# Kernel tuning notes

Hardware: AMD Instinct MI355X
Metric: run time of the kernel (lower is better)

## Reference

```python
import jax, jax.numpy as jnp
import numpy as np
from functools import partial

NUM_STEPS = 30  # Euler integration steps (inte_steps)


def _point_sample(vol, pts):
    """Trilinear sample of vol [C,D,H,W] at pts [N,3] (voxel coords, (d,h,w) order).
    Matches torch grid_sample(mode='bilinear', padding_mode='border', align_corners=True)
    after the normalize+flip done in PointPooling. Returns [C,N]."""
    dims = jnp.asarray(vol.shape[1:], dtype=pts.dtype)  # (D,H,W)
    p = jnp.clip(pts, 0.0, dims - 1.0)  # border padding == clamp coords
    p0 = jnp.floor(p)
    frac = p - p0  # [N,3]
    i0 = p0.astype(jnp.int32)
    i1 = jnp.minimum(i0 + 1, (dims - 1.0).astype(jnp.int32))
    d0, h0, w0 = i0[:, 0], i0[:, 1], i0[:, 2]
    d1, h1, w1 = i1[:, 0], i1[:, 1], i1[:, 2]
    fd, fh, fw = frac[:, 0], frac[:, 1], frac[:, 2]
    g = lambda d, h, w: vol[:, d, h, w]  # [C,N] gather
    c000, c001 = g(d0, h0, w0), g(d0, h0, w1)
    c010, c011 = g(d0, h1, w0), g(d0, h1, w1)
    c100, c101 = g(d1, h0, w0), g(d1, h0, w1)
    c110, c111 = g(d1, h1, w0), g(d1, h1, w1)
    c00 = c000 * (1 - fw) + c001 * fw
    c01 = c010 * (1 - fw) + c011 * fw
    c10 = c100 * (1 - fw) + c101 * fw
    c11 = c110 * (1 - fw) + c111 * fw
    c0 = c00 * (1 - fh) + c01 * fh
    c1 = c10 * (1 - fh) + c11 * fh
    return c0 * (1 - fd) + c1 * fd  # [C,N]


def _interp(flow, x):
    # flow [B,3,D,H,W], x [B,N,3] -> [B,N,3]
    out = jax.vmap(_point_sample)(flow, x)  # [B,3,N]
    return jnp.transpose(out, (0, 2, 1))


def _integrate_euler(flow, x, num_steps):
    flow = flow * (1.0 / num_steps)
    def step(x, _):
        return x + _interp(flow, x), None
    x, _ = jax.lax.scan(step, x, None, length=num_steps)
    return x


def _forward(verts, affine, flow_field):
    B, N, _ = verts.shape
    ones = jnp.ones((B, N, 1), dtype=verts.dtype)
    homog = jnp.concatenate([verts, ones], axis=-1)  # [B,N,4]
    pred = jnp.einsum('bij,bnj->bni', affine, homog)[..., :3]
    aux = _integrate_euler(flow_field, pred, NUM_STEPS)
    flow_int = aux - pred  # [B,N,3]
    pred = aux
    flow_int = jnp.transpose(flow_int, (0, 2, 1))[..., None, None]  # [B,3,N,1,1]
    homog2 = jnp.concatenate([pred, ones], axis=-1)
    inv_aff = jnp.linalg.inv(affine)
    pred = jnp.einsum('bij,bnj->bni', inv_aff, homog2)[..., :3]
    return pred, flow_int


def setup_inputs() -> dict:
    key = jax.random.key(0)
    k1, k2, k3 = jax.random.split(key, 3)
    B, N = 2, 140000
    D = H = W = 192
    dims = jnp.asarray([D - 1, H - 1, W - 1], dtype=jnp.float32)
    verts = jax.random.uniform(k1, (B, N, 3), dtype=jnp.float32) * dims
    affine = jnp.eye(4, dtype=jnp.float32)[None] + 0.01 * jax.random.normal(k2, (B, 4, 4), dtype=jnp.float32)
    flow_field = jax.random.normal(k3, (B, 3, D, H, W), dtype=jnp.float32)
    return {"verts": verts, "affine": affine, "flow_field": flow_field}


def reference(verts, affine, flow_field):
    return _forward(verts, affine, flow_field)
```

## Files before the change

### kernel.cpp

```cpp
#include <hip/hip_runtime.h>
#include <hip/hip_fp16.h>

#define NSTEPS 30
#define DIM 192
static constexpr long DHW = (long)DIM * DIM * DIM;
static constexpr int PTS_PER_WAVE = 21;

__global__ void invert4x4_kernel(const float* __restrict__ aff,
                                 float* __restrict__ out, int B) {
    int b = blockIdx.x * blockDim.x + threadIdx.x;
    if (b >= B) return;
    double a[16];
#pragma unroll
    for (int i = 0; i < 16; i++) a[i] = (double)aff[b * 16 + i];
    double s0 = a[0]*a[5]  - a[4]*a[1];
    double s1 = a[0]*a[6]  - a[4]*a[2];
    double s2 = a[0]*a[7]  - a[4]*a[3];
    double s3 = a[1]*a[6]  - a[5]*a[2];
    double s4 = a[1]*a[7]  - a[5]*a[3];
    double s5 = a[2]*a[7]  - a[6]*a[3];
    double c5 = a[10]*a[15] - a[14]*a[11];
    double c4 = a[9]*a[15]  - a[13]*a[11];
    double c3 = a[9]*a[14]  - a[13]*a[10];
    double c2 = a[8]*a[15]  - a[12]*a[11];
    double c1 = a[8]*a[14]  - a[12]*a[10];
    double c0 = a[8]*a[13]  - a[12]*a[9];
    double det = s0*c5 - s1*c4 + s2*c3 + s3*c2 - s4*c1 + s5*c0;
    double inv = 1.0 / det;
    double o[16];
    o[0]  = ( a[5]*c5 - a[6]*c4 + a[7]*c3) * inv;
    o[1]  = (-a[1]*c5 + a[2]*c4 - a[3]*c3) * inv;
    o[2]  = ( a[13]*s5 - a[14]*s4 + a[15]*s3) * inv;
    o[3]  = (-a[9]*s5 + a[10]*s4 - a[11]*s3) * inv;
    o[4]  = (-a[4]*c5 + a[6]*c2 - a[7]*c1) * inv;
    o[5]  = ( a[0]*c5 - a[2]*c2 + a[3]*c1) * inv;
    o[6]  = (-a[12]*s5 + a[14]*s2 - a[15]*s1) * inv;
    o[7]  = ( a[8]*s5 - a[10]*s2 + a[11]*s1) * inv;
    o[8]  = ( a[4]*c4 - a[5]*c2 + a[7]*c0) * inv;
    o[9]  = (-a[0]*c4 + a[1]*c2 - a[3]*c0) * inv;
    o[10] = ( a[12]*s4 - a[13]*s2 + a[15]*s0) * inv;
    o[11] = (-a[8]*s4 + a[9]*s2 - a[11]*s0) * inv;
    o[12] = (-a[4]*c3 + a[5]*c1 - a[6]*c0) * inv;
    o[13] = ( a[0]*c3 - a[1]*c1 + a[2]*c0) * inv;
    o[14] = (-a[12]*s3 + a[13]*s1 - a[14]*s0) * inv;
    o[15] = ( a[8]*s3 - a[9]*s1 + a[10]*s0) * inv;
#pragma unroll
    for (int i = 0; i < 16; i++) out[b * 16 + i] = (float)o[i];
}

__global__ __launch_bounds__(256) void repack4_kernel(const float* __restrict__ flow,
                                                      __half* __restrict__ packed) {
    long q = (long)blockIdx.x * blockDim.x + threadIdx.x;
    int b = blockIdx.y;
    long v0 = q * 4;
    if (v0 >= DHW) return;
    const float* F = flow + (size_t)b * 3 * DHW;
    float4 f0 = *reinterpret_cast<const float4*>(F + v0);
    float4 f1 = *reinterpret_cast<const float4*>(F + v0 + DHW);
    float4 f2 = *reinterpret_cast<const float4*>(F + v0 + 2 * DHW);
    union { __half2 h[2]; int2 i2; } u;
    int4 o0, o1;
    u.h[0] = __floats2half2_rn(f0.x, f1.x); u.h[1] = __floats2half2_rn(f2.x, 0.f);
    o0.x = u.i2.x; o0.y = u.i2.y;
    u.h[0] = __floats2half2_rn(f0.y, f1.y); u.h[1] = __floats2half2_rn(f2.y, 0.f);
    o0.z = u.i2.x; o0.w = u.i2.y;
    u.h[0] = __floats2half2_rn(f0.z, f1.z); u.h[1] = __floats2half2_rn(f2.z, 0.f);
    o1.x = u.i2.x; o1.y = u.i2.y;
    u.h[0] = __floats2half2_rn(f0.w, f1.w); u.h[1] = __floats2half2_rn(f2.w, 0.f);
    o1.z = u.i2.x; o1.w = u.i2.y;
    int4* out = reinterpret_cast<int4*>(packed) + (((size_t)b * DHW + v0) >> 1);
    out[0] = o0;
    out[1] = o1;
}

static __device__ __forceinline__ float2 h2f(unsigned u) {
    return __half22float2(__builtin_bit_cast(__half2, u));
}

__global__ __launch_bounds__(256) void deform1_kernel(
    const float* __restrict__ verts,
    const float* __restrict__ affine,
    const __half* __restrict__ packed,
    const float* __restrict__ invaff,
    float* __restrict__ out_pred,
    float* __restrict__ out_flow,
    int N, int B) {
    int idx = blockIdx.x * blockDim.x + threadIdx.x;
    int total = B * N;
    bool valid = idx < total;
    int i = valid ? idx : total - 1;
    int b = i / N;
    int n = i - b * N;

    const float* A = affine + b * 16;
    const float* v = verts + (size_t)i * 3;
    float vx = v[0], vy = v[1], vz = v[2];
    float x = A[0] * vx + A[1] * vy + A[2]  * vz + A[3];
    float y = A[4] * vx + A[5] * vy + A[6]  * vz + A[7];
    float z = A[8] * vx + A[9] * vy + A[10] * vz + A[11];
    const float px = x, py = y, pz = z;

    const char* Pb = (const char*)(packed + (size_t)b * DHW * 4);
    const float scale = (float)(1.0 / NSTEPS);

    float cc[3][8];
    int key = -1;

    for (int s = 0; s < NSTEPS; s++) {
        float pd = fminf(fmaxf(x, 0.0f), (float)(DIM - 1));
        float ph = fminf(fmaxf(y, 0.0f), (float)(DIM - 1));
        float pw = fminf(fmaxf(z, 0.0f), (float)(DIM - 1));
        float fd0 = floorf(pd), fh0 = floorf(ph), fw0 = floorf(pw);
        int d0 = (int)fd0, h0 = (int)fh0, w0 = (int)fw0;
        float fd = pd - fd0, fh = ph - fh0, fw = pw - fw0;

        int k = (d0 * DIM + h0) * DIM + w0;
        if (k != key) {
            key = k;
            int d1 = min(d0 + 1, DIM - 1);
            int h1 = min(h0 + 1, DIM - 1);
            int lb = min(w0, DIM - 2);
            int sel = w0 - lb;
            int rr[4];
            rr[0] = (d0 * DIM + h0) * DIM;
            rr[1] = (d0 * DIM + h1) * DIM;
            rr[2] = (d1 * DIM + h0) * DIM;
            rr[3] = (d1 * DIM + h1) * DIM;
#pragma unroll
            for (int r = 0; r < 4; r++) {
                const uint2* p = reinterpret_cast<const uint2*>(
                    Pb + (size_t)(rr[r] + lb) * 8);
                uint2 qa = p[0];
                uint2 qb = p[1];
                float2 a01 = h2f(qa.x), a2_ = h2f(qa.y);
                float2 b01 = h2f(qb.x), b2_ = h2f(qb.y);
                float c0a = sel ? b01.x : a01.x;
                float c1a = sel ? b01.y : a01.y;
                float c2a = sel ? b2_.x : a2_.x;
                cc[0][2*r+0] = c0a  * scale; cc[0][2*r+1] = b01.x * scale;
                cc[1][2*r+0] = c1a  * scale; cc[1][2*r+1] = b01.y * scale;
                cc[2][2*r+0] = c2a  * scale; cc[2][2*r+1] = b2_.x * scale;
            }
        }

        float omfw = 1.0f - fw, omfh = 1.0f - fh, omfd = 1.0f - fd;
        float vals[3];
#pragma unroll
        for (int c = 0; c < 3; c++) {
            float c00 = cc[c][0] * omfw + cc[c][1] * fw;
            float c01 = cc[c][2] * omfw + cc[c][3] * fw;
            float c10 = cc[c][4] * omfw + cc[c][5] * fw;
            float c11 = cc[c][6] * omfw + cc[c][7] * fw;
            float c0 = c00 * omfh + c01 * fh;
            float c1 = c10 * omfh + c11 * fh;
            vals[c] = c0 * omfd + c1 * fd;
        }
        x += vals[0];
        y += vals[1];
        z += vals[2];
    }

    if (valid) {
        float fx = x - px, fy = y - py, fz = z - pz;
        const float* Ai = invaff + b * 16;
        float ox = Ai[0] * x + Ai[1] * y + Ai[2]  * z + Ai[3];
        float oy = Ai[4] * x + Ai[5] * y + Ai[6]  * z + Ai[7];
        float oz = Ai[8] * x + Ai[9] * y + Ai[10] * z + Ai[11];
        size_t po = (size_t)i * 3;
        out_pred[po + 0] = ox;
        out_pred[po + 1] = oy;
        out_pred[po + 2] = oz;
        size_t fo = (size_t)b * 3 * N + n;
        out_flow[fo]         = fx;
        out_flow[fo + N]     = fy;
        out_flow[fo + 2 * N] = fz;
    }
}

__global__ __launch_bounds__(256) void deform_kernel(
    const float* __restrict__ verts,
    const float* __restrict__ affine,
    const float* __restrict__ flow,
    const float* __restrict__ invaff,
    float* __restrict__ out_pred,
    float* __restrict__ out_flow,
    int N, int B) {
    int lane = threadIdx.x & 63;
    int wib  = threadIdx.x >> 6;
    long gwave = (long)blockIdx.x * (blockDim.x >> 6) + wib;
    int piw = lane / 3;
    if (piw > PTS_PER_WAVE - 1) piw = PTS_PER_WAVE - 1;
    int ch = lane - piw * 3;
    if (ch > 2) ch = 2;
    long pt = gwave * PTS_PER_WAVE + piw;
    bool valid = (lane < 63) && (pt < (long)B * N);
    long ptc = valid ? pt : ((long)B * N - 1);
    int b = (int)(ptc / N);
    int n = (int)(ptc - (long)b * N);
    const float* A = affine + b * 16;
    const float* v = verts + (size_t)ptc * 3;
    float vx = v[0], vy = v[1], vz = v[2];
    float x = A[0] * vx + A[1] * vy + A[2]  * vz + A[3];
    float y = A[4] * vx + A[5] * vy + A[6]  * vz + A[7];
    float z = A[8] * vx + A[9] * vy + A[10] * vz + A[11];
    float p0 = (ch == 0) ? x : (ch == 1) ? y : z;
    const float* Fc = flow + ((size_t)b * 3 + ch) * (size_t)DHW;
    const float scale = (float)(1.0 / NSTEPS);
    float cc[8];
    int key = -1;
    int bl = piw * 3;
    for (int s = 0; s < NSTEPS; s++) {
        float pd = fminf(fmaxf(x, 0.0f), (float)(DIM - 1));
        float ph = fminf(fmaxf(y, 0.0f), (float)(DIM - 1));
        float pw = fminf(fmaxf(z, 0.0f), (float)(DIM - 1));
        float fd0 = floorf(pd), fh0 = floorf(ph), fw0 = floorf(pw);
        int d0 = (int)fd0, h0 = (int)fh0, w0 = (int)fw0;
        float fd = pd - fd0, fh = ph - fh0, fw = pw - fw0;
        int k = (d0 * DIM + h0) * DIM + w0;
        if (k != key) {
            key = k;
            int d1 = min(d0 + 1, DIM - 1);
            int h1 = min(h0 + 1, DIM - 1);
            int w1 = min(w0 + 1, DIM - 1);
            int r00 = (d0 * DIM + h0) * DIM;
            int r01 = (d0 * DIM + h1) * DIM;
            int r10 = (d1 * DIM + h0) * DIM;
            int r11 = (d1 * DIM + h1) * DIM;
            cc[0] = Fc[r00 + w0] * scale;
            cc[1] = Fc[r00 + w1] * scale;
            cc[2] = Fc[r01 + w0] * scale;
            cc[3] = Fc[r01 + w1] * scale;
            cc[4] = Fc[r10 + w0] * scale;
            cc[5] = Fc[r10 + w1] * scale;
            cc[6] = Fc[r11 + w0] * scale;
            cc[7] = Fc[r11 + w1] * scale;
        }
        float omfw = 1.0f - fw, omfh = 1.0f - fh, omfd = 1.0f - fd;
        float c00 = cc[0] * omfw + cc[1] * fw;
        float c01 = cc[2] * omfw + cc[3] * fw;
        float c10 = cc[4] * omfw + cc[5] * fw;
        float c11 = cc[6] * omfw + cc[7] * fw;
        float c0 = c00 * omfh + c01 * fh;
        float c1 = c10 * omfh + c11 * fh;
        float val = c0 * omfd + c1 * fd;
        float v0 = __shfl(val, bl,     64);
        float v1 = __shfl(val, bl + 1, 64);
        float v2 = __shfl(val, bl + 2, 64);
        x += v0; y += v1; z += v2;
    }
    if (valid) {
        float posc = (ch == 0) ? x : (ch == 1) ? y : z;
        float fint = posc - p0;
        const float* Ai = invaff + b * 16 + ch * 4;
        float o = Ai[0] * x + Ai[1] * y + Ai[2] * z + Ai[3];
        out_pred[(size_t)ptc * 3 + ch] = o;
        out_flow[(size_t)b * 3 * N + (size_t)ch * N + n] = fint;
    }
}

extern "C" void kernel_launch(void* const* d_in, const int* in_sizes, int n_in,
                              void* d_out, int out_size, void* d_ws, size_t ws_size,
                              hipStream_t stream) {
    const float* verts  = (const float*)d_in[0];
    const float* affine = (const float*)d_in[1];
    const float* flow   = (const float*)d_in[2];

    int B = in_sizes[1] / 16;
    int N = in_sizes[0] / (3 * B);

    float* out_pred = (float*)d_out;
    float* out_flow = out_pred + (size_t)B * N * 3;

    size_t packed_bytes = (size_t)B * DHW * 4 * sizeof(__half);
    bool use_packed = (ws_size >= packed_bytes + 256);

    int total = B * N;

    if (use_packed) {
        __half* packed = (__half*)d_ws;
        float* invaff  = (float*)((char*)d_ws + packed_bytes);
        hipLaunchKernelGGL(invert4x4_kernel, dim3(1), dim3(64), 0, stream,
                           affine, invaff, B);
        long quads = (DHW + 3) / 4;
        long vblocks = (quads + 255) / 256;
        hipLaunchKernelGGL(repack4_kernel, dim3((unsigned)vblocks, B), dim3(256), 0,
                           stream, flow, packed);
        int blocks = (total + 255) / 256;
        hipLaunchKernelGGL(deform1_kernel, dim3(blocks), dim3(256), 0, stream,
                           verts, affine, packed, invaff, out_pred, out_flow, N, B);
    } else {
        float* invaff = (float*)d_ws;
        hipLaunchKernelGGL(invert4x4_kernel, dim3(1), dim3(64), 0, stream,
                           affine, invaff, B);
        long waves  = ((long)total + PTS_PER_WAVE - 1) / PTS_PER_WAVE;
        long blocks = (waves + 3) / 4;
        hipLaunchKernelGGL(deform_kernel, dim3((unsigned)blocks), dim3(256), 0,
                           stream, verts, affine, flow, invaff,
                           out_pred, out_flow, N, B);
    }
}
```

Baseline: 327.2 us.

## Split each point's trilinear gather across four lanes with shuffle reduction

Each point is now handled by four lanes, each loading one of the four (d,h) corner rows of the packed fp16 flow. Each lane computes its weighted w-interpolation, and the partial sums are combined with xor-shuffles. This cuts per-thread dependent gather latency and register use, and spreads the memory requests over more threads. In exchange it launches four times as many threads, repeats the position math redundantly, adds shuffle overhead on every step, and makes the cache-key skip decide per lane.

```diff
diff --git a/kernel.cpp b/kernel.cpp
--- a/kernel.cpp
+++ b/kernel.cpp
@@ -77,7 +77,7 @@
     return __half22float2(__builtin_bit_cast(__half2, u));
 }
 
-__global__ __launch_bounds__(256) void deform1_kernel(
+__global__ __launch_bounds__(256) void deform4_kernel(
     const float* __restrict__ verts,
     const float* __restrict__ affine,
     const __half* __restrict__ packed,
@@ -85,12 +85,16 @@
     float* __restrict__ out_pred,
     float* __restrict__ out_flow,
     int N, int B) {
-    int idx = blockIdx.x * blockDim.x + threadIdx.x;
-    int total = B * N;
-    bool valid = idx < total;
-    int i = valid ? idx : total - 1;
-    int b = i / N;
-    int n = i - b * N;
+    long t = (long)blockIdx.x * blockDim.x + threadIdx.x;
+    long total = (long)B * N;
+    long pt = t >> 2;
+    int sub = (int)(t & 3);
+    bool valid = pt < total;
+    long i = valid ? pt : total - 1;
+    int b = (int)(i / N);
+    int n = (int)(i - (long)b * N);
+    int hsel = sub & 1;
+    int dsel = (sub >> 1) & 1;
 
     const float* A = affine + b * 16;
     const float* v = verts + (size_t)i * 3;
@@ -103,7 +107,7 @@
     const char* Pb = (const char*)(packed + (size_t)b * DHW * 4);
     const float scale = (float)(1.0 / NSTEPS);
 
-    float cc[3][8];
+    float cw0[3], cw1[3];
     int key = -1;
 
     for (int s = 0; s < NSTEPS; s++) {
@@ -119,61 +123,43 @@
             key = k;
             int d1 = min(d0 + 1, DIM - 1);
             int h1 = min(h0 + 1, DIM - 1);
+            int dr = dsel ? d1 : d0;
+            int hr = hsel ? h1 : h0;
             int lb = min(w0, DIM - 2);
             int sel = w0 - lb;
-            int rr[4];
-            rr[0] = (d0 * DIM + h0) * DIM;
-            rr[1] = (d0 * DIM + h1) * DIM;
-            rr[2] = (d1 * DIM + h0) * DIM;
-            rr[3] = (d1 * DIM + h1) * DIM;
-#pragma unroll
-            for (int r = 0; r < 4; r++) {
-                const uint2* p = reinterpret_cast<const uint2*>(
-                    Pb + (size_t)(rr[r] + lb) * 8);
-                uint2 qa = p[0];
-                uint2 qb = p[1];
-                float2 a01 = h2f(qa.x), a2_ = h2f(qa.y);
-                float2 b01 = h2f(qb.x), b2_ = h2f(qb.y);
-                float c0a = sel ? b01.x : a01.x;
-                float c1a = sel ? b01.y : a01.y;
-                float c2a = sel ? b2_.x : a2_.x;
-                cc[0][2*r+0] = c0a  * scale; cc[0][2*r+1] = b01.x * scale;
-                cc[1][2*r+0] = c1a  * scale; cc[1][2*r+1] = b01.y * scale;
-                cc[2][2*r+0] = c2a  * scale; cc[2][2*r+1] = b2_.x * scale;
-            }
+            const uint2* p = reinterpret_cast<const uint2*>(
+                Pb + (size_t)((dr * DIM + hr) * DIM + lb) * 8);
+            uint2 qa = p[0];
+            uint2 qb = p[1];
+            float2 a01 = h2f(qa.x), a2_ = h2f(qa.y);
+            float2 b01 = h2f(qb.x), b2_ = h2f(qb.y);
+            cw0[0] = (sel ? b01.x : a01.x) * scale;
+            cw0[1] = (sel ? b01.y : a01.y) * scale;
+            cw0[2] = (sel ? b2_.x : a2_.x) * scale;
+            cw1[0] = b01.x * scale;
+            cw1[1] = b01.y * scale;
+            cw1[2] = b2_.x * scale;
         }
 
-        float omfw = 1.0f - fw, omfh = 1.0f - fh, omfd = 1.0f - fd;
-        float vals[3];
-#pragma unroll
-        for (int c = 0; c < 3; c++) {
-            float c00 = cc[c][0] * omfw + cc[c][1] * fw;
-            float c01 = cc[c][2] * omfw + cc[c][3] * fw;
-            float c10 = cc[c][4] * omfw + cc[c][5] * fw;
-            float c11 = cc[c][6] * omfw + cc[c][7] * fw;
-            float c0 = c00 * omfh + c01 * fh;
-            float c1 = c10 * omfh + c11 * fh;
-            vals[c] = c0 * omfd + c1 * fd;
-        }
-        x += vals[0];
-        y += vals[1];
-        z += vals[2];
-    }
-
-    if (valid) {
-        float fx = x - px, fy = y - py, fz = z - pz;
-        const float* Ai = invaff + b * 16;
-        float ox = Ai[0] * x + Ai[1] * y + Ai[2]  * z + Ai[3];
-        float oy = Ai[4] * x + Ai[5] * y + Ai[6]  * z + Ai[7];
-        float oz = Ai[8] * x + Ai[9] * y + Ai[10] * z + Ai[11];
-        size_t po = (size_t)i * 3;
-        out_pred[po + 0] = ox;
-        out_pred[po + 1] = oy;
-        out_pred[po + 2] = oz;
-        size_t fo = (size_t)b * 3 * N + n;
-        out_flow[fo]         = fx;
-        out_flow[fo + N]     = fy;
-        out_flow[fo + 2 * N] = fz;
+        float omfw = 1.0f - fw;
+        float wgt = (hsel ? fh : 1.0f - fh) * (dsel ? fd : 1.0f - fd);
+        float v0 = (cw0[0] * omfw + cw1[0] * fw) * wgt;
+        float v1 = (cw0[1] * omfw + cw1[1] * fw) * wgt;
+        float v2 = (cw0[2] * omfw + cw1[2] * fw) * wgt;
+        v0 += __shfl_xor(v0, 1, 64); v0 += __shfl_xor(v0, 2, 64);
+        v1 += __shfl_xor(v1, 1, 64); v1 += __shfl_xor(v1, 2, 64);
+        v2 += __shfl_xor(v2, 1, 64); v2 += __shfl_xor(v2, 2, 64);
+        x += v0; y += v1; z += v2;
+    }
+
+    if (valid && sub < 3) {
+        float posc = (sub == 0) ? x : (sub == 1) ? y : z;
+        float p0c  = (sub == 0) ? px : (sub == 1) ? py : pz;
+        float fint = posc - p0c;
+        const float* Ai = invaff + b * 16 + sub * 4;
+        float o = Ai[0] * x + Ai[1] * y + Ai[2] * z + Ai[3];
+        out_pred[(size_t)i * 3 + sub] = o;
+        out_flow[(size_t)b * 3 * N + (size_t)sub * N + n] = fint;
     }
 }
 
@@ -274,7 +260,7 @@
     size_t packed_bytes = (size_t)B * DHW * 4 * sizeof(__half);
     bool use_packed = (ws_size >= packed_bytes + 256);
 
-    int total = B * N;
+    long total = (long)B * N;
 
     if (use_packed) {
         __half* packed = (__half*)d_ws;
@@ -285,14 +271,16 @@
         long vblocks = (quads + 255) / 256;
         hipLaunchKernelGGL(repack4_kernel, dim3((unsigned)vblocks, B), dim3(256), 0,
                            stream, flow, packed);
-        int blocks = (total + 255) / 256;
-        hipLaunchKernelGGL(deform1_kernel, dim3(blocks), dim3(256), 0, stream,
-                           verts, affine, packed, invaff, out_pred, out_flow, N, B);
+        long threads = total * 4;
+        long blocks = (threads + 255) / 256;
+        hipLaunchKernelGGL(deform4_kernel, dim3((unsigned)blocks), dim3(256), 0,
+                           stream, verts, affine, packed, invaff,
+                           out_pred, out_flow, N, B);
     } else {
         float* invaff = (float*)d_ws;
         hipLaunchKernelGGL(invert4x4_kernel, dim3(1), dim3(64), 0, stream,
                            affine, invaff, B);
-        long waves  = ((long)total + PTS_PER_WAVE - 1) / PTS_PER_WAVE;
+        long waves  = (total + PTS_PER_WAVE - 1) / PTS_PER_WAVE;
         long blocks = (waves + 3) / 4;
         hipLaunchKernelGGL(deform_kernel, dim3((unsigned)blocks), dim3(256), 0,
                            stream, verts, affine, flow, invaff,
```

After: 315.6 us. 3.5% less time.
